# Kernel optimization log

Measured on AMD Instinct MI355X. Metric: run time of the kernel, lower is better.

## Reference

```python
import jax, jax.numpy as jnp
import numpy as np

L, B, D, A, H = 128, 128, 1024, 1024, 2048  # src_len, batch, dec_hid, align, enc_hid


def setup_inputs() -> dict:
    key = jax.random.key(0)
    ks = jax.random.split(key, 8)
    s_tm1 = jax.random.normal(ks[0], (B, D), dtype=jnp.float32)
    xs_h = jax.random.normal(ks[1], (L, B, H), dtype=jnp.float32)
    uh = jax.random.normal(ks[2], (L, B, A), dtype=jnp.float32)
    xs_mask = jnp.ones((L, B), dtype=jnp.float32)
    # learned params: sa = Linear(D -> A), a1 = Linear(A -> 1)
    W_sa = jax.random.normal(ks[3], (A, D), dtype=jnp.float32) * 0.02
    b_sa = jnp.zeros((A,), dtype=jnp.float32)
    w_a1 = jax.random.normal(ks[4], (A,), dtype=jnp.float32) * 0.02
    b_a1 = jnp.zeros((), dtype=jnp.float32)
    return {"s_tm1": s_tm1, "xs_h": xs_h, "uh": uh, "xs_mask": xs_mask,
            "W_sa": W_sa, "b_sa": b_sa, "w_a1": w_a1, "b_a1": b_a1}


def reference(s_tm1, xs_h, uh, xs_mask, W_sa, b_sa, w_a1, b_a1):
    # sa(s_tm1): (B, A), broadcast over L against uh (L, B, A)
    proj = s_tm1 @ W_sa.T + b_sa
    h = jnp.tanh(proj[None, :, :] + uh)            # (L, B, A)
    # a1: (L, B, A) . (A,) -> (L, B); exp (no max-subtraction, faithful to source)
    e_ij = jnp.exp(jnp.einsum('lba,a->lb', h, w_a1) + b_a1)
    e_ij = e_ij * xs_mask
    e_ij = e_ij / e_ij.sum(axis=0, keepdims=True)  # normalize over source length
    attend = jnp.einsum('lb,lbh->bh', e_ij, xs_h)  # (B, H)
    return e_ij, attend
```

## Files before the change

### kernel.cpp

```cpp
#include <hip/hip_runtime.h>

#define L_DIM 128
#define B_DIM 128
#define D_DIM 1024
#define A_DIM 1024
#define H_DIM 2048
#define KSPLIT 16

__global__ __launch_bounds__(256) void k1_gemm_part(const float* __restrict__ s_tm1,
                                                    const float* __restrict__ W_sa,
                                                    float* __restrict__ proj_part) {
    __shared__ float sWT[64][68];
    __shared__ float sST[64][68];
    const int a0 = blockIdx.x * 64;
    const int b0 = blockIdx.y * 64;
    const int kc = blockIdx.z;
    const int k0 = kc * 64;
    const int t  = threadIdx.x;

    {
        const int c = (t & 15) * 4;
        const int r = t >> 4;
#pragma unroll
        for (int p = 0; p < 4; ++p) {
            const int row = r + p * 16;
            float4 w4 = *(const float4*)(W_sa + (size_t)(a0 + row) * D_DIM + k0 + c);
            sWT[c + 0][row] = w4.x; sWT[c + 1][row] = w4.y;
            sWT[c + 2][row] = w4.z; sWT[c + 3][row] = w4.w;
            float4 s4 = *(const float4*)(s_tm1 + (size_t)(b0 + row) * D_DIM + k0 + c);
            sST[c + 0][row] = s4.x; sST[c + 1][row] = s4.y;
            sST[c + 2][row] = s4.z; sST[c + 3][row] = s4.w;
        }
    }
    __syncthreads();

    const int tx = t & 15;
    const int ty = t >> 4;
    float acc[4][4] = {};
#pragma unroll 4
    for (int d = 0; d < 64; ++d) {
        float4 av = *(const float4*)&sWT[d][tx * 4];
        float4 bv = *(const float4*)&sST[d][ty * 4];
        float a_[4] = {av.x, av.y, av.z, av.w};
        float b_[4] = {bv.x, bv.y, bv.z, bv.w};
#pragma unroll
        for (int j = 0; j < 4; ++j)
#pragma unroll
            for (int i = 0; i < 4; ++i)
                acc[j][i] += a_[i] * b_[j];
    }

    float* base = proj_part + (size_t)kc * B_DIM * A_DIM;
#pragma unroll
    for (int j = 0; j < 4; ++j)
#pragma unroll
        for (int i = 0; i < 4; ++i)
            base[(size_t)(b0 + ty * 4 + j) * A_DIM + a0 + tx * 4 + i] = acc[j][i];
}

__global__ __launch_bounds__(256) void k1_reduce(const float* __restrict__ proj_part,
                                                 float* __restrict__ proj) {
    const size_t i4 = (size_t)blockIdx.x * 256 + threadIdx.x;
    const float4* pp = (const float4*)proj_part;
    float4 acc = pp[i4];
#pragma unroll
    for (int kc = 1; kc < KSPLIT; ++kc) {
        float4 v = pp[(size_t)kc * (B_DIM * A_DIM / 4) + i4];
        acc.x += v.x; acc.y += v.y; acc.z += v.z; acc.w += v.w;
    }
    ((float4*)proj)[i4] = acc;
}

__device__ __forceinline__ float tanh_fast(float x) {
    float e = __expf(2.0f * x);
    return (e - 1.0f) * __builtin_amdgcn_rcpf(e + 1.0f);
}

__global__ __launch_bounds__(256) void k2_logits(const float* __restrict__ uh,
                                                 const float* __restrict__ proj,
                                                 const float* __restrict__ b_sa,
                                                 const float* __restrict__ w_a1,
                                                 const float* __restrict__ b_a1,
                                                 const float* __restrict__ mask,
                                                 float* __restrict__ e_raw) {
    const int wave = threadIdx.x >> 6;
    const int lane = threadIdx.x & 63;
    const int flat = blockIdx.x * 4 + wave;
    const int b    = flat & (B_DIM - 1);

    const float* up = uh   + (size_t)flat * A_DIM;
    const float* pp = proj + (size_t)b    * A_DIM;

    float acc = 0.0f;
#pragma unroll
    for (int c = 0; c < 4; ++c) {
        const int off = c * 256 + lane * 4;
        float4 u = *(const float4*)(up + off);
        float4 p = *(const float4*)(pp + off);
        float4 s = *(const float4*)(b_sa + off);
        float4 w = *(const float4*)(w_a1 + off);
        acc += tanh_fast(u.x + p.x + s.x) * w.x;
        acc += tanh_fast(u.y + p.y + s.y) * w.y;
        acc += tanh_fast(u.z + p.z + s.z) * w.z;
        acc += tanh_fast(u.w + p.w + s.w) * w.w;
    }
#pragma unroll
    for (int off = 32; off > 0; off >>= 1)
        acc += __shfl_down(acc, off);
    if (lane == 0)
        e_raw[flat] = __expf(acc + b_a1[0]) * mask[flat];
}

__global__ __launch_bounds__(256) void k3_attend(const float* __restrict__ e_raw,
                                                 const float* __restrict__ xs_h,
                                                 float* __restrict__ out_e,
                                                 float* __restrict__ out_att) {
    __shared__ float se[L_DIM];
    __shared__ float s_inv;
    const int b     = blockIdx.y;
    const int chunk = blockIdx.x;
    const int t     = threadIdx.x;

    if (t < L_DIM) se[t] = e_raw[t * B_DIM + b];
    __syncthreads();
    if (t < 64) {
        float v = se[t] + se[t + 64];
#pragma unroll
        for (int off = 32; off > 0; off >>= 1)
            v += __shfl_down(v, off);
        if (t == 0) s_inv = 1.0f / v;
    }
    __syncthreads();
    if (t < L_DIM) se[t] *= s_inv;
    __syncthreads();
    if (chunk == 0 && t < L_DIM) out_e[t * B_DIM + b] = se[t];

    const int h0 = chunk * 512 + t * 2;
    const float* xp = xs_h + (size_t)b * H_DIM + h0;
    float accx = 0.0f, accy = 0.0f;
#pragma unroll 8
    for (int l = 0; l < L_DIM; ++l) {
        float  w = se[l];
        float2 x = *(const float2*)(xp + (size_t)l * (B_DIM * H_DIM));
        accx += w * x.x;
        accy += w * x.y;
    }
    float* op = out_att + (size_t)b * H_DIM + h0;
    op[0] = accx;
    op[1] = accy;
}

extern "C" void kernel_launch(void* const* d_in, const int* in_sizes, int n_in,
                              void* d_out, int out_size, void* d_ws, size_t ws_size,
                              hipStream_t stream) {
    const float* s_tm1 = (const float*)d_in[0];
    const float* xs_h  = (const float*)d_in[1];
    const float* uh    = (const float*)d_in[2];
    const float* mask  = (const float*)d_in[3];
    const float* W_sa  = (const float*)d_in[4];
    const float* b_sa  = (const float*)d_in[5];
    const float* w_a1  = (const float*)d_in[6];
    const float* b_a1  = (const float*)d_in[7];

    float* proj_part = (float*)d_ws;
    float* proj      = proj_part + (size_t)KSPLIT * B_DIM * A_DIM;
    float* e_raw     = proj + (size_t)B_DIM * A_DIM;

    float* out_e   = (float*)d_out;
    float* out_att = out_e + L_DIM * B_DIM;

    k1_gemm_part<<<dim3(A_DIM / 64, B_DIM / 64, KSPLIT), 256, 0, stream>>>(
        s_tm1, W_sa, proj_part);
    k1_reduce<<<dim3(B_DIM * A_DIM / 4 / 256), 256, 0, stream>>>(proj_part, proj);
    k2_logits<<<dim3(L_DIM * B_DIM / 4), 256, 0, stream>>>(uh, proj, b_sa, w_a1,
                                                           b_a1, mask, e_raw);
    k3_attend<<<dim3(H_DIM / 512, B_DIM), 256, 0, stream>>>(e_raw, xs_h,
                                                            out_e, out_att);
}
```

Measured before the change: 257.2 us.

## Rewrite tanh-weighted sum via reciprocal identity, fold bias into projection, widen attend grid

The logits kernel now uses the identity tanh(x)=1-2/(e^{2x}+1). That turns each element into one exp2 and one reciprocal, with no subtract or multiply. The constant sum of w_a1 plus b_a1 is folded into a scalar computed once in the reduce kernel. The reduce kernel also pre-adds b_sa and pre-scales the projection by 2*log2(e), which drops the b_sa load and some ALU work from the hot loop. The attend kernel switches from two floats per thread to one, doubling the block count, and uses two accumulators for more memory-level parallelism. The trade-off is narrower scalar loads in the attend kernel and slightly different rounding behaviour.

After: 257.4 us. About the same (+0.1%).

```diff
diff --git a/kernel.cpp b/kernel.cpp
--- a/kernel.cpp
+++ b/kernel.cpp
@@ -6,6 +6,9 @@
 #define A_DIM 1024
 #define H_DIM 2048
 #define KSPLIT 16
+
+#define KC 2.8853900817779268f
+#define LOG2E 1.4426950408889634f
 
 __global__ __launch_bounds__(256) void k1_gemm_part(const float* __restrict__ s_tm1,
                                                     const float* __restrict__ W_sa,
@@ -59,7 +62,12 @@
 }
 
 __global__ __launch_bounds__(256) void k1_reduce(const float* __restrict__ proj_part,
-                                                 float* __restrict__ proj) {
+                                                 const float* __restrict__ b_sa,
+                                                 const float* __restrict__ w_a1,
+                                                 const float* __restrict__ b_a1,
+                                                 float* __restrict__ proj2,
+                                                 float* __restrict__ c0) {
+    __shared__ float sw[4];
     const size_t i4 = (size_t)blockIdx.x * 256 + threadIdx.x;
     const float4* pp = (const float4*)proj_part;
     float4 acc = pp[i4];
@@ -68,19 +76,30 @@
         float4 v = pp[(size_t)kc * (B_DIM * A_DIM / 4) + i4];
         acc.x += v.x; acc.y += v.y; acc.z += v.z; acc.w += v.w;
     }
-    ((float4*)proj)[i4] = acc;
-}
-
-__device__ __forceinline__ float tanh_fast(float x) {
-    float e = __expf(2.0f * x);
-    return (e - 1.0f) * __builtin_amdgcn_rcpf(e + 1.0f);
+    const int a4 = (int)(i4 & (A_DIM / 4 - 1));
+    float4 bs = ((const float4*)b_sa)[a4];
+    float4 o;
+    o.x = (acc.x + bs.x) * KC; o.y = (acc.y + bs.y) * KC;
+    o.z = (acc.z + bs.z) * KC; o.w = (acc.w + bs.w) * KC;
+    ((float4*)proj2)[i4] = o;
+
+    if (blockIdx.x == 0) {
+        float4 w4 = ((const float4*)w_a1)[threadIdx.x];
+        float s = w4.x + w4.y + w4.z + w4.w;
+#pragma unroll
+        for (int off = 32; off > 0; off >>= 1)
+            s += __shfl_down(s, off);
+        if ((threadIdx.x & 63) == 0) sw[threadIdx.x >> 6] = s;
+        __syncthreads();
+        if (threadIdx.x == 0)
+            c0[0] = (sw[0] + sw[1] + sw[2] + sw[3] + b_a1[0]) * LOG2E;
+    }
 }
 
 __global__ __launch_bounds__(256) void k2_logits(const float* __restrict__ uh,
-                                                 const float* __restrict__ proj,
-                                                 const float* __restrict__ b_sa,
+                                                 const float* __restrict__ proj2,
                                                  const float* __restrict__ w_a1,
-                                                 const float* __restrict__ b_a1,
+                                                 const float* __restrict__ c0p,
                                                  const float* __restrict__ mask,
                                                  float* __restrict__ e_raw) {
     const int wave = threadIdx.x >> 6;
@@ -88,27 +107,31 @@
     const int flat = blockIdx.x * 4 + wave;
     const int b    = flat & (B_DIM - 1);
 
-    const float* up = uh   + (size_t)flat * A_DIM;
-    const float* pp = proj + (size_t)b    * A_DIM;
-
-    float acc = 0.0f;
+    const float* up = uh    + (size_t)flat * A_DIM;
+    const float* pp = proj2 + (size_t)b    * A_DIM;
+
+    float acc0 = 0.0f, acc1 = 0.0f;
 #pragma unroll
     for (int c = 0; c < 4; ++c) {
         const int off = c * 256 + lane * 4;
         float4 u = *(const float4*)(up + off);
         float4 p = *(const float4*)(pp + off);
-        float4 s = *(const float4*)(b_sa + off);
         float4 w = *(const float4*)(w_a1 + off);
-        acc += tanh_fast(u.x + p.x + s.x) * w.x;
-        acc += tanh_fast(u.y + p.y + s.y) * w.y;
-        acc += tanh_fast(u.z + p.z + s.z) * w.z;
-        acc += tanh_fast(u.w + p.w + s.w) * w.w;
-    }
+        float e0 = __builtin_amdgcn_exp2f(fmaf(u.x, KC, p.x));
+        float e1 = __builtin_amdgcn_exp2f(fmaf(u.y, KC, p.y));
+        float e2 = __builtin_amdgcn_exp2f(fmaf(u.z, KC, p.z));
+        float e3 = __builtin_amdgcn_exp2f(fmaf(u.w, KC, p.w));
+        acc0 = fmaf(w.x, __builtin_amdgcn_rcpf(e0 + 1.0f), acc0);
+        acc1 = fmaf(w.y, __builtin_amdgcn_rcpf(e1 + 1.0f), acc1);
+        acc0 = fmaf(w.z, __builtin_amdgcn_rcpf(e2 + 1.0f), acc0);
+        acc1 = fmaf(w.w, __builtin_amdgcn_rcpf(e3 + 1.0f), acc1);
+    }
+    float acc = acc0 + acc1;
 #pragma unroll
     for (int off = 32; off > 0; off >>= 1)
         acc += __shfl_down(acc, off);
     if (lane == 0)
-        e_raw[flat] = __expf(acc + b_a1[0]) * mask[flat];
+        e_raw[flat] = __builtin_amdgcn_exp2f(fmaf(acc, -KC, c0p[0])) * mask[flat];
 }
 
 __global__ __launch_bounds__(256) void k3_attend(const float* __restrict__ e_raw,
@@ -135,19 +158,15 @@
     __syncthreads();
     if (chunk == 0 && t < L_DIM) out_e[t * B_DIM + b] = se[t];
 
-    const int h0 = chunk * 512 + t * 2;
+    const int h0 = chunk * 256 + t;
     const float* xp = xs_h + (size_t)b * H_DIM + h0;
-    float accx = 0.0f, accy = 0.0f;
+    float a0 = 0.0f, a1 = 0.0f;
 #pragma unroll 8
-    for (int l = 0; l < L_DIM; ++l) {
-        float  w = se[l];
-        float2 x = *(const float2*)(xp + (size_t)l * (B_DIM * H_DIM));
-        accx += w * x.x;
-        accy += w * x.y;
-    }
-    float* op = out_att + (size_t)b * H_DIM + h0;
-    op[0] = accx;
-    op[1] = accy;
+    for (int l = 0; l < L_DIM; l += 2) {
+        a0 = fmaf(se[l],     xp[(size_t)l       * (B_DIM * H_DIM)], a0);
+        a1 = fmaf(se[l + 1], xp[(size_t)(l + 1) * (B_DIM * H_DIM)], a1);
+    }
+    out_att[(size_t)b * H_DIM + h0] = a0 + a1;
 }
 
 extern "C" void kernel_launch(void* const* d_in, const int* in_sizes, int n_in,
@@ -163,17 +182,19 @@
     const float* b_a1  = (const float*)d_in[7];
 
     float* proj_part = (float*)d_ws;
-    float* proj      = proj_part + (size_t)KSPLIT * B_DIM * A_DIM;
-    float* e_raw     = proj + (size_t)B_DIM * A_DIM;
+    float* proj2     = proj_part + (size_t)KSPLIT * B_DIM * A_DIM;
+    float* e_raw     = proj2 + (size_t)B_DIM * A_DIM;
+    float* c0        = e_raw + (size_t)L_DIM * B_DIM;
 
     float* out_e   = (float*)d_out;
     float* out_att = out_e + L_DIM * B_DIM;
 
     k1_gemm_part<<<dim3(A_DIM / 64, B_DIM / 64, KSPLIT), 256, 0, stream>>>(
         s_tm1, W_sa, proj_part);
-    k1_reduce<<<dim3(B_DIM * A_DIM / 4 / 256), 256, 0, stream>>>(proj_part, proj);
-    k2_logits<<<dim3(L_DIM * B_DIM / 4), 256, 0, stream>>>(uh, proj, b_sa, w_a1,
-                                                           b_a1, mask, e_raw);
-    k3_attend<<<dim3(H_DIM / 512, B_DIM), 256, 0, stream>>>(e_raw, xs_h,
+    k1_reduce<<<dim3(B_DIM * A_DIM / 4 / 256), 256, 0, stream>>>(
+        proj_part, b_sa, w_a1, b_a1, proj2, c0);
+    k2_logits<<<dim3(L_DIM * B_DIM / 4), 256, 0, stream>>>(uh, proj2, w_a1,
+                                                           c0, mask, e_raw);
+    k3_attend<<<dim3(H_DIM / 256, B_DIM), 256, 0, stream>>>(e_raw, xs_h,
                                                             out_e, out_att);
 }
```
